# Performance work log

Measured on AMD Instinct MI355X. Metric: run time of the kernel, lower is better.

The kernel has to match this reference:

```python
import jax, jax.numpy as jnp
import numpy as np

TOKENS, N_EMBD, N_EXPERTS, TOP_K = 16384, 4096, 64, 2


def setup_inputs() -> dict:
    key = jax.random.key(0)
    k_x, k_n, k_wr, k_br, k_wn, k_bn = jax.random.split(key, 6)
    s = 1.0 / np.sqrt(N_EMBD)
    return {
        "x": jax.random.normal(k_x, (TOKENS, N_EMBD), dtype=jnp.float32),
        "noise": jax.random.normal(k_n, (TOKENS, N_EXPERTS), dtype=jnp.float32),
        "route_w": jax.random.uniform(k_wr, (N_EXPERTS, N_EMBD), jnp.float32, -s, s),
        "route_b": jax.random.uniform(k_br, (N_EXPERTS,), jnp.float32, -s, s),
        "noise_w": jax.random.uniform(k_wn, (N_EXPERTS, N_EMBD), jnp.float32, -s, s),
        "noise_b": jax.random.uniform(k_bn, (N_EXPERTS,), jnp.float32, -s, s),
    }


def reference(x, noise, route_w, route_b, noise_w, noise_b):
    # logits, noise_logits: [tokens, n_experts]
    logits = jnp.einsum("td,ed->te", x, route_w) + route_b
    noise_logits = jnp.einsum("td,ed->te", x, noise_w) + noise_b
    # noisy logits (computed as in original; not used in output, matching source)
    top_k_noisy_logits = noise_logits + noise * jax.nn.softplus(noise_logits)
    # top-k on the CLEAN logits (as in source), scatter into -inf, softmax
    top_k_logits, indices = jax.lax.top_k(logits, TOP_K)  # [tokens, k]
    neg_inf = jnp.full_like(top_k_noisy_logits, -jnp.inf)
    rows = jnp.arange(logits.shape[0])[:, None]
    sparse_logits = neg_inf.at[rows, indices].set(top_k_logits)
    router_output = jax.nn.softmax(sparse_logits, axis=-1)
    return router_output, indices
```

## Files before the change

kernel.cpp:

```cpp
#include <hip/hip_runtime.h>
#include <math.h>


#define TOKENS 16384
#define EMB    4096
#define NE     64
#define TB     32
#define NWAVES 8
#define KQ     (EMB / NWAVES)
#define KR     8
#define NSEG   (KQ / KR)

#define GLOAD_LDS16(g, l)                                                      \
    __builtin_amdgcn_global_load_lds(                                          \
        (const __attribute__((address_space(1))) void*)(g),                    \
        (__attribute__((address_space(3))) void*)(l), 16, 0, 0)

__global__ __launch_bounds__(256) void wt4_prep_kernel(const float* __restrict__ w,
                                                       float* __restrict__ wt4) {
    int idx = blockIdx.x * 256 + threadIdx.x;
    int k   = idx >> 6;
    int col = idx & 63;
    int le  = col >> 2;
    int m   = col & 3;
    wt4[idx] = w[(le + 16 * m) * EMB + k];
}

__global__ __launch_bounds__(512, 4) void router_kernel(const float* __restrict__ x,
                                                        const float* __restrict__ wt4,
                                                        const float* __restrict__ rb,
                                                        float* __restrict__ out) {
    __shared__ float smem[8192];

    const int tid  = threadIdx.x;
    const int lane = tid & 63;
    const int wq   = __builtin_amdgcn_readfirstlane(tid >> 6);
    const long tok0 = (long)blockIdx.x * TB;

    const int g  = lane >> 4;
    const int le = lane & 15;
    const int swz   = g << 4;
    const int tbase = g * 256;

    const int r_  = lane >> 1;
    const int hl  = lane & 1;
    const int t_s = r_ ^ ((r_ >> 4) & 1);
    const int h_s = hl ^ ((r_ >> 3) & 1);
    const float* xsrc = x + (tok0 + t_s) * (long)EMB + wq * KQ + 4 * h_s;

    const float* wsrc = wt4 + (long)(wq * KQ) * NE + le * 4;

    float acc[8][4];
#pragma unroll
    for (int i = 0; i < 8; ++i)
#pragma unroll
        for (int m = 0; m < 4; ++m) acc[i][m] = 0.f;

    float* lds0 = &smem[wq * 512];
    float* lds1 = &smem[wq * 512 + 256];

    GLOAD_LDS16(xsrc, lds0);

    auto compute_seg = [&](const float* __restrict__ wseg,
                           const char* __restrict__ xb) {
        float w4a[KR][4];
#pragma unroll
        for (int k = 0; k < KR; ++k)
            *reinterpret_cast<float4*>(&w4a[k][0]) =
                *reinterpret_cast<const float4*>(wseg + k * NE);
#pragma unroll
        for (int i = 0; i < 8; ++i) {
            const float4 xa = *reinterpret_cast<const float4*>(xb + ((tbase + i * 32 + 0)  ^ swz));
            const float4 xc = *reinterpret_cast<const float4*>(xb + ((tbase + i * 32 + 16) ^ swz));
#pragma unroll
            for (int m = 0; m < 4; ++m) {
                float a = acc[i][m];
                a = fmaf(xa.x, w4a[0][m], a);
                a = fmaf(xa.y, w4a[1][m], a);
                a = fmaf(xa.z, w4a[2][m], a);
                a = fmaf(xa.w, w4a[3][m], a);
                a = fmaf(xc.x, w4a[4][m], a);
                a = fmaf(xc.y, w4a[5][m], a);
                a = fmaf(xc.z, w4a[6][m], a);
                a = fmaf(xc.w, w4a[7][m], a);
                acc[i][m] = a;
            }
        }
    };

    for (int s = 0; s < NSEG - 1; ++s) {
        const int b = s & 1;
        GLOAD_LDS16(xsrc + (s + 1) * KR, (b ? lds0 : lds1));
        asm volatile("s_waitcnt vmcnt(1)" ::: "memory");
        compute_seg(wsrc + (long)s * KR * NE,
                    (const char*)(b ? lds1 : lds0));
    }
    {
        const int b = (NSEG - 1) & 1;
        asm volatile("s_waitcnt vmcnt(0)" ::: "memory");
        compute_seg(wsrc + (long)(NSEG - 1) * KR * NE,
                    (const char*)(b ? lds1 : lds0));
    }

    __syncthreads();
    if (wq >= 4) {
#pragma unroll
        for (int i = 0; i < 8; ++i)
#pragma unroll
            for (int m = 0; m < 4; ++m)
                smem[((wq & 3) * 32 + g * 8 + i) * 64 + le + 16 * m] = acc[i][m];
    }
    __syncthreads();
    if (wq < 4) {
#pragma unroll
        for (int i = 0; i < 8; ++i)
#pragma unroll
            for (int m = 0; m < 4; ++m) {
                const int idx = ((wq & 3) * 32 + g * 8 + i) * 64 + le + 16 * m;
                smem[idx] += acc[i][m];
            }
    }
    __syncthreads();
    {
        const int t  = tid >> 4;
        const int e0 = (tid & 15) * 4;
        float4 sum = *reinterpret_cast<const float4*>(rb + e0);
#pragma unroll
        for (int r = 0; r < 4; ++r) {
            const float4 p = *reinterpret_cast<const float4*>(&smem[(r * 32 + t) * 64 + e0]);
            sum.x += p.x; sum.y += p.y; sum.z += p.z; sum.w += p.w;
        }
        *reinterpret_cast<float4*>(&smem[t * 64 + e0]) = sum;
    }
    __syncthreads();

    if (tid < TB) {
        const int t = tid;
        float m1 = -INFINITY, m2 = -INFINITY;
        int i1 = 0, i2 = 0;
        for (int e = 0; e < NE; ++e) {
            float v = smem[t * 64 + e];
            if (v > m1)      { m2 = m1; i2 = i1; m1 = v; i1 = e; }
            else if (v > m2) { m2 = v;  i2 = e; }
        }
        const float ed = expf(m2 - m1);
        const float p1 = 1.f / (1.f + ed);
        smem[2048 + t]      = p1;
        smem[2048 + 32 + t] = 1.f - p1;
        smem[2048 + 64 + t] = (float)i1;
        smem[2048 + 96 + t] = (float)i2;
    }
    __syncthreads();

    {
        const int t  = tid >> 4;
        const int e0 = (tid & 15) * 4;
        const int i1 = (int)smem[2048 + 64 + t];
        const int i2 = (int)smem[2048 + 96 + t];
        const float p1 = smem[2048 + t];
        const float p2 = smem[2048 + 32 + t];
        float v[4];
#pragma unroll
        for (int j = 0; j < 4; ++j) {
            const int e = e0 + j;
            v[j] = (e == i1) ? p1 : ((e == i2) ? p2 : 0.f);
        }
        *reinterpret_cast<float4*>(out + (tok0 + t) * NE + e0) =
            make_float4(v[0], v[1], v[2], v[3]);
    }
    if (tid < TB) {
        float* idxo = out + (long)TOKENS * NE + (tok0 + tid) * 2;
        idxo[0] = smem[2048 + 64 + tid];
        idxo[1] = smem[2048 + 96 + tid];
    }
}

extern "C" void kernel_launch(void* const* d_in, const int* in_sizes, int n_in,
                              void* d_out, int out_size, void* d_ws, size_t ws_size,
                              hipStream_t stream) {
    const float* x       = (const float*)d_in[0];
    const float* route_w = (const float*)d_in[2];
    const float* route_b = (const float*)d_in[3];
    float* wt4 = (float*)d_ws;
    float* out = (float*)d_out;

    hipLaunchKernelGGL(wt4_prep_kernel, dim3((EMB * NE) / 256), dim3(256), 0, stream,
                       route_w, wt4);
    hipLaunchKernelGGL(router_kernel, dim3(TOKENS / TB), dim3(512), 0, stream,
                       x, wt4, route_b, out);
}
```

Baseline: 158.6 us.

## Halve tokens per block and restructure LDS x tiling with 16-wide k chunks

Reduces tokens per block from 32 to 16, doubling the grid to 1024 blocks, and halves the per-thread accumulator tile. The x staging is reworked so each 16-byte global-to-LDS load covers 16 k-values for 16 tokens, with an XOR swizzle on the column chunk, and each stage runs two 8-wide weight segments. The aim is more blocks and less register pressure for better occupancy and wave balance on the memory-bound GEMV. The cost is that each weight fragment is reused across half as many tokens, so weight traffic per token doubles.

```diff
diff --git a/kernel.cpp b/kernel.cpp
--- a/kernel.cpp
+++ b/kernel.cpp
@@ -5,11 +5,10 @@
 #define TOKENS 16384
 #define EMB    4096
 #define NE     64
-#define TB     32
+#define TB     16
 #define NWAVES 8
 #define KQ     (EMB / NWAVES)
-#define KR     8
-#define NSEG   (KQ / KR)
+#define NPAIR  (KQ / 16)
 
 #define GLOAD_LDS16(g, l)                                                      \
     __builtin_amdgcn_global_load_lds(                                          \
@@ -30,7 +29,7 @@
                                                         const float* __restrict__ wt4,
                                                         const float* __restrict__ rb,
                                                         float* __restrict__ out) {
-    __shared__ float smem[8192];
+    __shared__ float smem[4096];
 
     const int tid  = threadIdx.x;
     const int lane = tid & 63;
@@ -39,95 +38,93 @@
 
     const int g  = lane >> 4;
     const int le = lane & 15;
-    const int swz   = g << 4;
-    const int tbase = g * 256;
 
-    const int r_  = lane >> 1;
-    const int hl  = lane & 1;
-    const int t_s = r_ ^ ((r_ >> 4) & 1);
-    const int h_s = hl ^ ((r_ >> 3) & 1);
-    const float* xsrc = x + (tok0 + t_s) * (long)EMB + wq * KQ + 4 * h_s;
+    const int t_s = lane >> 2;
+    const int c_s = (lane & 3) ^ ((lane >> 4) & 3);
+    const float* xsrc = x + (tok0 + t_s) * (long)EMB + wq * KQ + c_s * 4;
 
     const float* wsrc = wt4 + (long)(wq * KQ) * NE + le * 4;
 
-    float acc[8][4];
+    float acc[4][4];
 #pragma unroll
-    for (int i = 0; i < 8; ++i)
+    for (int i = 0; i < 4; ++i)
 #pragma unroll
         for (int m = 0; m < 4; ++m) acc[i][m] = 0.f;
 
     float* lds0 = &smem[wq * 512];
     float* lds1 = &smem[wq * 512 + 256];
 
-    GLOAD_LDS16(xsrc, lds0);
-
-    auto compute_seg = [&](const float* __restrict__ wseg,
-                           const char* __restrict__ xb) {
-        float w4a[KR][4];
+    auto seg8 = [&](const float* __restrict__ wp, const char* __restrict__ xb,
+                    const int c0) {
+        float w4a[8][4];
 #pragma unroll
-        for (int k = 0; k < KR; ++k)
+        for (int k = 0; k < 8; ++k)
             *reinterpret_cast<float4*>(&w4a[k][0]) =
-                *reinterpret_cast<const float4*>(wseg + k * NE);
+                *reinterpret_cast<const float4*>(wp + k * NE);
 #pragma unroll
-        for (int i = 0; i < 8; ++i) {
-            const float4 xa = *reinterpret_cast<const float4*>(xb + ((tbase + i * 32 + 0)  ^ swz));
-            const float4 xc = *reinterpret_cast<const float4*>(xb + ((tbase + i * 32 + 16) ^ swz));
+        for (int cc = 0; cc < 2; ++cc) {
+            const int c = c0 + cc;
 #pragma unroll
-            for (int m = 0; m < 4; ++m) {
-                float a = acc[i][m];
-                a = fmaf(xa.x, w4a[0][m], a);
-                a = fmaf(xa.y, w4a[1][m], a);
-                a = fmaf(xa.z, w4a[2][m], a);
-                a = fmaf(xa.w, w4a[3][m], a);
-                a = fmaf(xc.x, w4a[4][m], a);
-                a = fmaf(xc.y, w4a[5][m], a);
-                a = fmaf(xc.z, w4a[6][m], a);
-                a = fmaf(xc.w, w4a[7][m], a);
-                acc[i][m] = a;
+            for (int i = 0; i < 4; ++i) {
+                const float4 xv = *reinterpret_cast<const float4*>(
+                    xb + i * 64 + ((c ^ g) * 16));
+#pragma unroll
+                for (int m = 0; m < 4; ++m) {
+                    float a = acc[i][m];
+                    a = fmaf(xv.x, w4a[cc * 4 + 0][m], a);
+                    a = fmaf(xv.y, w4a[cc * 4 + 1][m], a);
+                    a = fmaf(xv.z, w4a[cc * 4 + 2][m], a);
+                    a = fmaf(xv.w, w4a[cc * 4 + 3][m], a);
+                    acc[i][m] = a;
+                }
             }
         }
     };
 
-    for (int s = 0; s < NSEG - 1; ++s) {
-        const int b = s & 1;
-        GLOAD_LDS16(xsrc + (s + 1) * KR, (b ? lds0 : lds1));
+    GLOAD_LDS16(xsrc, lds0);
+
+    for (int p = 0; p < NPAIR - 1; ++p) {
+        const int b = p & 1;
+        GLOAD_LDS16(xsrc + (p + 1) * 16, (b ? lds0 : lds1));
         asm volatile("s_waitcnt vmcnt(1)" ::: "memory");
-        compute_seg(wsrc + (long)s * KR * NE,
-                    (const char*)(b ? lds1 : lds0));
+        const char* xb = (const char*)(b ? lds1 : lds0) + g * 256;
+        seg8(wsrc + (long)(p * 16 + 0) * NE, xb, 0);
+        seg8(wsrc + (long)(p * 16 + 8) * NE, xb, 2);
     }
     {
-        const int b = (NSEG - 1) & 1;
+        const int b = (NPAIR - 1) & 1;
         asm volatile("s_waitcnt vmcnt(0)" ::: "memory");
-        compute_seg(wsrc + (long)(NSEG - 1) * KR * NE,
-                    (const char*)(b ? lds1 : lds0));
+        const char* xb = (const char*)(b ? lds1 : lds0) + g * 256;
+        seg8(wsrc + (long)((NPAIR - 1) * 16 + 0) * NE, xb, 0);
+        seg8(wsrc + (long)((NPAIR - 1) * 16 + 8) * NE, xb, 2);
     }
 
     __syncthreads();
     if (wq >= 4) {
 #pragma unroll
-        for (int i = 0; i < 8; ++i)
+        for (int i = 0; i < 4; ++i)
 #pragma unroll
             for (int m = 0; m < 4; ++m)
-                smem[((wq & 3) * 32 + g * 8 + i) * 64 + le + 16 * m] = acc[i][m];
+                smem[((wq & 3) * 16 + g * 4 + i) * 64 + le + 16 * m] = acc[i][m];
     }
     __syncthreads();
     if (wq < 4) {
 #pragma unroll
-        for (int i = 0; i < 8; ++i)
+        for (int i = 0; i < 4; ++i)
 #pragma unroll
             for (int m = 0; m < 4; ++m) {
-                const int idx = ((wq & 3) * 32 + g * 8 + i) * 64 + le + 16 * m;
+                const int idx = ((wq & 3) * 16 + g * 4 + i) * 64 + le + 16 * m;
                 smem[idx] += acc[i][m];
             }
     }
     __syncthreads();
-    {
+    if (tid < 256) {
         const int t  = tid >> 4;
         const int e0 = (tid & 15) * 4;
         float4 sum = *reinterpret_cast<const float4*>(rb + e0);
 #pragma unroll
         for (int r = 0; r < 4; ++r) {
-            const float4 p = *reinterpret_cast<const float4*>(&smem[(r * 32 + t) * 64 + e0]);
+            const float4 p = *reinterpret_cast<const float4*>(&smem[(r * 16 + t) * 64 + e0]);
             sum.x += p.x; sum.y += p.y; sum.z += p.z; sum.w += p.w;
         }
         *reinterpret_cast<float4*>(&smem[t * 64 + e0]) = sum;
@@ -145,20 +142,20 @@
         }
         const float ed = expf(m2 - m1);
         const float p1 = 1.f / (1.f + ed);
-        smem[2048 + t]      = p1;
-        smem[2048 + 32 + t] = 1.f - p1;
-        smem[2048 + 64 + t] = (float)i1;
-        smem[2048 + 96 + t] = (float)i2;
+        smem[1024 + t]      = p1;
+        smem[1024 + 16 + t] = 1.f - p1;
+        smem[1024 + 32 + t] = (float)i1;
+        smem[1024 + 48 + t] = (float)i2;
     }
     __syncthreads();
 
-    {
+    if (tid < 256) {
         const int t  = tid >> 4;
         const int e0 = (tid & 15) * 4;
-        const int i1 = (int)smem[2048 + 64 + t];
-        const int i2 = (int)smem[2048 + 96 + t];
-        const float p1 = smem[2048 + t];
-        const float p2 = smem[2048 + 32 + t];
+        const int i1 = (int)smem[1024 + 32 + t];
+        const int i2 = (int)smem[1024 + 48 + t];
+        const float p1 = smem[1024 + t];
+        const float p2 = smem[1024 + 16 + t];
         float v[4];
 #pragma unroll
         for (int j = 0; j < 4; ++j) {
@@ -170,8 +167,8 @@
     }
     if (tid < TB) {
         float* idxo = out + (long)TOKENS * NE + (tok0 + tid) * 2;
-        idxo[0] = smem[2048 + 64 + tid];
-        idxo[1] = smem[2048 + 96 + tid];
+        idxo[0] = smem[1024 + 32 + tid];
+        idxo[1] = smem[1024 + 48 + tid];
     }
 }
 
```

After: 169.0 us. +6.6%, slower.
